# Optimization experiments

Measured on AMD Instinct MI355X. Metric: run time of the kernel, lower is better.

## Reference

```python
import jax, jax.numpy as jnp
import numpy as np

N_DETS = 50000
DEG = 32
N_EDGES = N_DETS * DEG

def _xavier(key, fan_in, fan_out):
    lim = np.sqrt(6.0 / (fan_in + fan_out)).astype(np.float32)
    return jax.random.uniform(key, (fan_in, fan_out), jnp.float32, -lim, lim)

def setup_inputs() -> dict:
    key = jax.random.key(0)
    ks = jax.random.split(key, 10)
    detFeatures = jax.random.normal(ks[0], (N_DETS, 128), jnp.float32)
    # every detection has exactly DEG neighbor pairs -> sorted segment ids, no empty segments
    cIdxs = jnp.repeat(jnp.arange(N_DETS, dtype=jnp.int64), DEG)
    nIdxs = jax.random.randint(ks[1], (N_EDGES,), 0, N_DETS, jnp.int64)
    pairFeatures = jax.random.normal(ks[2], (N_EDGES, 32), jnp.float32)
    return {
        "detFeatures": detFeatures,
        "cIdxs": cIdxs,
        "nIdxs": nIdxs,
        "pairFeatures": pairFeatures,
        "W_fc1": _xavier(ks[3], 128, 32), "b_fc1": jnp.zeros((32,), jnp.float32),
        "W_pw1": _xavier(ks[4], 96, 64), "b_pw1": jnp.zeros((64,), jnp.float32),
        "W_pw2": _xavier(ks[5], 64, 64), "b_pw2": jnp.zeros((64,), jnp.float32),
        "W_pm1": _xavier(ks[6], 64, 64), "b_pm1": jnp.zeros((64,), jnp.float32),
        "W_pm2": _xavier(ks[7], 64, 64), "b_pm2": jnp.zeros((64,), jnp.float32),
        "W_out": _xavier(ks[8], 64, 128), "b_out": jnp.zeros((128,), jnp.float32),
    }

def reference(detFeatures, cIdxs, nIdxs, pairFeatures,
              W_fc1, b_fc1, W_pw1, b_pw1, W_pw2, b_pw2,
              W_pm1, b_pm1, W_pm2, b_pm2, W_out, b_out):
    relu = jax.nn.relu
    # fc1: [N,128] -> [N,32]
    h = relu(detFeatures @ W_fc1 + b_fc1)
    # gather center / neighbor feats per pair; zero neighbor feats on identity rows
    cFeats = h[cIdxs]                                   # [E,32]
    nFeats = jnp.where((cIdxs == nIdxs)[:, None], 0.0, h[nIdxs])  # [E,32]
    x = jnp.concatenate((pairFeatures, cFeats, nFeats), axis=1)   # [E,96]
    x = relu(x @ W_pw1 + b_pw1)                         # [E,64]
    x = relu(x @ W_pw2 + b_pw2)                         # [E,64]
    # per-detection segment max (replaces the O(N) python loop)
    m = jax.ops.segment_max(x, cIdxs, num_segments=detFeatures.shape[0])  # [N,64]
    m = relu(m @ W_pm1 + b_pm1)
    m = relu(m @ W_pm2 + b_pm2)
    refined = m @ W_out + b_out                         # [N,128]
    return relu(detFeatures + refined)
```

## Files before the change

kernel.cpp:

```cpp
#include <hip/hip_runtime.h>

#define NDET 50000
#define DEG 32
#define NEDGE (NDET * DEG)
#define NGROUP (NEDGE / 64)

typedef __attribute__((ext_vector_type(8))) short short8;
typedef __attribute__((ext_vector_type(4))) float f32x4;

__device__ inline unsigned short f2bf(float x) {
    return (unsigned short)((__builtin_bit_cast(unsigned int, x) + 0x8000u) >> 16);
}

__device__ inline short8 pack8(float4 a, float4 b) {
    short8 r;
    r[0] = (short)f2bf(a.x); r[1] = (short)f2bf(a.y);
    r[2] = (short)f2bf(a.z); r[3] = (short)f2bf(a.w);
    r[4] = (short)f2bf(b.x); r[5] = (short)f2bf(b.y);
    r[6] = (short)f2bf(b.z); r[7] = (short)f2bf(b.w);
    return r;
}

__global__ __launch_bounds__(256, 4) void fc1_kernel(
    const float* __restrict__ detF,
    const float* __restrict__ W,
    const float* __restrict__ b,
    unsigned short* __restrict__ hbf)
{
    __shared__ __align__(16) unsigned short WT[32 * 136];

    const int tid  = threadIdx.x;
    const int lane = tid & 63;
    const int wv   = tid >> 6;
    const int m16  = lane & 15;
    const int q    = lane >> 4;

    for (int i = tid; i < 32 * 128; i += 256) {
        int n = i >> 7, k = i & 127;
        WT[n * 136 + k] = f2bf(W[k * 32 + n]);
    }
    __syncthreads();

    const int g = blockIdx.x * 4 + wv;
    if (g >= (NDET + 63) / 64) return;
    const int d0 = g * 64;

    f32x4 acc[4][2];
#pragma unroll
    for (int nt = 0; nt < 2; nt++) {
        float c0 = b[nt * 16 + m16];
#pragma unroll
        for (int mt = 0; mt < 4; mt++) acc[mt][nt] = (f32x4){c0, c0, c0, c0};
    }

#pragma unroll
    for (int ks = 0; ks < 4; ks++) {
#pragma unroll
        for (int mt = 0; mt < 4; mt++) {
            int row = d0 + mt * 16 + m16;
            if (row >= NDET) row = NDET - 1;
            const float* pr = detF + (size_t)row * 128 + ks * 32 + q * 8;
            short8 a = pack8(*(const float4*)pr, *(const float4*)(pr + 4));
#pragma unroll
            for (int nt = 0; nt < 2; nt++) {
                short8 bf = *(const short8*)&WT[(nt * 16 + m16) * 136 + ks * 32 + q * 8];
                acc[mt][nt] = __builtin_amdgcn_mfma_f32_16x16x32_bf16(a, bf, acc[mt][nt], 0, 0, 0);
            }
        }
    }

#pragma unroll
    for (int mt = 0; mt < 4; mt++)
#pragma unroll
        for (int r = 0; r < 4; r++) {
            int row = d0 + mt * 16 + q * 4 + r;
            if (row < NDET) {
#pragma unroll
                for (int nt = 0; nt < 2; nt++)
                    hbf[(size_t)row * 32 + nt * 16 + m16] = f2bf(fmaxf(acc[mt][nt][r], 0.0f));
            }
        }
}

__global__ __launch_bounds__(256, 3) void edge_kernel(
    const unsigned short* __restrict__ hbf,
    const int* __restrict__ nIdx,
    const float* __restrict__ pairF,
    const float* __restrict__ W1,
    const float* __restrict__ b1,
    const float* __restrict__ W2,
    const float* __restrict__ b2,
    unsigned short* __restrict__ m_bf)
{
    __shared__ __align__(16) unsigned short Y1s[4][64 * 72];
    __shared__ __align__(16) unsigned short W2T[64 * 72];

    const int tid  = threadIdx.x;
    const int lane = tid & 63;
    const int wv   = tid >> 6;
    const int m16  = lane & 15;
    const int q    = lane >> 4;

    unsigned short* st = &Y1s[0][0];
    for (int i = tid; i < 64 * 96; i += 256) {
        int n = i / 96, k = i - n * 96;
        st[i] = f2bf(W1[k * 64 + n]);
    }
    for (int i = tid; i < 64 * 64; i += 256) {
        int n = i >> 6, k = i & 63;
        W2T[n * 72 + k] = f2bf(W2[k * 64 + n]);
    }
    __syncthreads();

    short8 w1f[3][4];
#pragma unroll
    for (int nt = 0; nt < 4; nt++) {
        const unsigned short* base = &st[(nt * 16 + m16) * 96];
        w1f[0][nt] = *(const short8*)&base[q * 8];
        w1f[1][nt] = *(const short8*)&base[64 + q * 8];
        w1f[2][nt] = *(const short8*)&base[32 + q * 8];
    }
    float b1r[4], b2r[4];
#pragma unroll
    for (int nt = 0; nt < 4; nt++) {
        b1r[nt] = b1[nt * 16 + m16];
        b2r[nt] = b2[nt * 16 + m16];
    }
    __syncthreads();

    unsigned short* Y1w = &Y1s[wv][0];

    const int wstride = (int)gridDim.x * 4;
    int g = blockIdx.x * 4 + wv;
    if (g >= NGROUP) return;

    int    ni[4];
    float4 pv[4][2];
    short8 nb[4];
    short8 cf2[2];

#define PREF(gg)                                                                  \
    {                                                                             \
        const int E0p = (gg) * 64, d0p = (gg) * 2;                                \
        _Pragma("unroll")                                                         \
        for (int mt = 0; mt < 4; mt++) {                                          \
            int e = E0p + mt * 16 + m16;                                          \
            ni[mt] = nIdx[e];                                                     \
            const float* pr = pairF + (size_t)e * 32 + q * 8;                     \
            pv[mt][0] = *(const float4*)pr;                                       \
            pv[mt][1] = *(const float4*)(pr + 4);                                 \
            nb[mt] = *(const short8*)&hbf[(size_t)ni[mt] * 32 + q * 8];           \
        }                                                                         \
        cf2[0] = *(const short8*)&hbf[(size_t)d0p * 32 + q * 8];                  \
        cf2[1] = *(const short8*)&hbf[(size_t)(d0p + 1) * 32 + q * 8];            \
    }

    PREF(g);
    const short8 zr = {0, 0, 0, 0, 0, 0, 0, 0};

    while (true) {
        const int d0 = g * 2;
        short8 ap[4], an[4], ac[4];
#pragma unroll
        for (int mt = 0; mt < 4; mt++) {
            ap[mt] = pack8(pv[mt][0], pv[mt][1]);
            an[mt] = (ni[mt] == d0 + (mt >> 1)) ? zr : nb[mt];
            ac[mt] = cf2[mt >> 1];
        }
        const int gn = g + wstride;
        const bool more = (gn < NGROUP);
        PREF(more ? gn : g);

        f32x4 acc[4][4];
#pragma unroll
        for (int mt = 0; mt < 4; mt++)
#pragma unroll
            for (int nt = 0; nt < 4; nt++) {
                float c0 = b1r[nt];
                acc[mt][nt] = (f32x4){c0, c0, c0, c0};
            }
#pragma unroll
        for (int mt = 0; mt < 4; mt++)
#pragma unroll
            for (int nt = 0; nt < 4; nt++) {
                acc[mt][nt] = __builtin_amdgcn_mfma_f32_16x16x32_bf16(ap[mt], w1f[0][nt], acc[mt][nt], 0, 0, 0);
                acc[mt][nt] = __builtin_amdgcn_mfma_f32_16x16x32_bf16(an[mt], w1f[1][nt], acc[mt][nt], 0, 0, 0);
                acc[mt][nt] = __builtin_amdgcn_mfma_f32_16x16x32_bf16(ac[mt], w1f[2][nt], acc[mt][nt], 0, 0, 0);
            }

#pragma unroll
        for (int mt = 0; mt < 4; mt++)
#pragma unroll
            for (int nt = 0; nt < 4; nt++)
#pragma unroll
                for (int r = 0; r < 4; r++)
                    Y1w[(mt * 16 + q * 4 + r) * 72 + nt * 16 + m16] =
                        f2bf(fmaxf(acc[mt][nt][r], 0.0f));

        f32x4 acc2[4][4];
#pragma unroll
        for (int mt = 0; mt < 4; mt++)
#pragma unroll
            for (int nt = 0; nt < 4; nt++) {
                float c0 = b2r[nt];
                acc2[mt][nt] = (f32x4){c0, c0, c0, c0};
            }
#pragma unroll
        for (int ks = 0; ks < 2; ks++) {
            short8 af[4];
#pragma unroll
            for (int mt = 0; mt < 4; mt++)
                af[mt] = *(const short8*)&Y1w[(mt * 16 + m16) * 72 + ks * 32 + q * 8];
#pragma unroll
            for (int nt = 0; nt < 4; nt++) {
                short8 wf = *(const short8*)&W2T[(nt * 16 + m16) * 72 + ks * 32 + q * 8];
#pragma unroll
                for (int mt = 0; mt < 4; mt++)
                    acc2[mt][nt] = __builtin_amdgcn_mfma_f32_16x16x32_bf16(af[mt], wf, acc2[mt][nt], 0, 0, 0);
            }
        }

#pragma unroll
        for (int d = 0; d < 2; d++)
#pragma unroll
            for (int nt = 0; nt < 4; nt++) {
                float v = 0.0f;
#pragma unroll
                for (int mt = 2 * d; mt < 2 * d + 2; mt++)
#pragma unroll
                    for (int r = 0; r < 4; r++) v = fmaxf(v, acc2[mt][nt][r]);
                v = fmaxf(v, __shfl_xor(v, 16));
                v = fmaxf(v, __shfl_xor(v, 32));
                if (q == 0) m_bf[(size_t)(d0 + d) * 64 + nt * 16 + m16] = f2bf(v);
            }

        if (!more) break;
        g = gn;
    }
#undef PREF
}

__global__ __launch_bounds__(256, 2) void tail_kernel(
    const float* __restrict__ detF,
    const unsigned short* __restrict__ m_bf,
    const float* __restrict__ Wm1, const float* __restrict__ bm1,
    const float* __restrict__ Wm2, const float* __restrict__ bm2,
    const float* __restrict__ Wo,  const float* __restrict__ bo,
    float* __restrict__ out)
{
    __shared__ __align__(16) unsigned short W1T[64 * 72];
    __shared__ __align__(16) unsigned short W2T[64 * 72];
    __shared__ __align__(16) unsigned short WoT[128 * 72];
    __shared__ __align__(16) unsigned short Tt[4][64 * 72];

    const int tid  = threadIdx.x;
    const int lane = tid & 63;
    const int wv   = tid >> 6;
    const int m16  = lane & 15;
    const int q    = lane >> 4;

    for (int i = tid; i < 64 * 64; i += 256) {
        int n = i >> 6, k = i & 63;
        W1T[n * 72 + k] = f2bf(Wm1[k * 64 + n]);
        W2T[n * 72 + k] = f2bf(Wm2[k * 64 + n]);
    }
    for (int i = tid; i < 128 * 64; i += 256) {
        int n = i >> 6, k = i & 63;
        WoT[n * 72 + k] = f2bf(Wo[k * 128 + n]);
    }
    __syncthreads();

    float bm1r[4], bm2r[4], bor[8];
#pragma unroll
    for (int nt = 0; nt < 4; nt++) {
        bm1r[nt] = bm1[nt * 16 + m16];
        bm2r[nt] = bm2[nt * 16 + m16];
    }
#pragma unroll
    for (int nt = 0; nt < 8; nt++) bor[nt] = bo[nt * 16 + m16];

    unsigned short* Tw = &Tt[wv][0];
    const int NTG = (NDET + 63) / 64;

    for (int gI = blockIdx.x * 4 + wv; gI < NTG; gI += (int)gridDim.x * 4) {
        const int d0 = gI * 64;

        f32x4 acc[4][4];
#pragma unroll
        for (int mt = 0; mt < 4; mt++)
#pragma unroll
            for (int nt = 0; nt < 4; nt++) {
                float c0 = bm1r[nt];
                acc[mt][nt] = (f32x4){c0, c0, c0, c0};
            }
#pragma unroll
        for (int ks = 0; ks < 2; ks++) {
            short8 af[4];
#pragma unroll
            for (int mt = 0; mt < 4; mt++) {
                int row = d0 + mt * 16 + m16;
                if (row >= NDET) row = NDET - 1;
                af[mt] = *(const short8*)&m_bf[(size_t)row * 64 + ks * 32 + q * 8];
            }
#pragma unroll
            for (int mt = 0; mt < 4; mt++)
#pragma unroll
                for (int nt = 0; nt < 4; nt++) {
                    short8 bf = *(const short8*)&W1T[(nt * 16 + m16) * 72 + ks * 32 + q * 8];
                    acc[mt][nt] = __builtin_amdgcn_mfma_f32_16x16x32_bf16(af[mt], bf, acc[mt][nt], 0, 0, 0);
                }
        }
#pragma unroll
        for (int mt = 0; mt < 4; mt++)
#pragma unroll
            for (int nt = 0; nt < 4; nt++)
#pragma unroll
                for (int r = 0; r < 4; r++)
                    Tw[(mt * 16 + q * 4 + r) * 72 + nt * 16 + m16] =
                        f2bf(fmaxf(acc[mt][nt][r], 0.0f));

#pragma unroll
        for (int mt = 0; mt < 4; mt++)
#pragma unroll
            for (int nt = 0; nt < 4; nt++) {
                float c0 = bm2r[nt];
                acc[mt][nt] = (f32x4){c0, c0, c0, c0};
            }
#pragma unroll
        for (int ks = 0; ks < 2; ks++) {
            short8 af[4];
#pragma unroll
            for (int mt = 0; mt < 4; mt++)
                af[mt] = *(const short8*)&Tw[(mt * 16 + m16) * 72 + ks * 32 + q * 8];
#pragma unroll
            for (int mt = 0; mt < 4; mt++)
#pragma unroll
                for (int nt = 0; nt < 4; nt++) {
                    short8 bf = *(const short8*)&W2T[(nt * 16 + m16) * 72 + ks * 32 + q * 8];
                    acc[mt][nt] = __builtin_amdgcn_mfma_f32_16x16x32_bf16(af[mt], bf, acc[mt][nt], 0, 0, 0);
                }
        }
#pragma unroll
        for (int mt = 0; mt < 4; mt++)
#pragma unroll
            for (int nt = 0; nt < 4; nt++)
#pragma unroll
                for (int r = 0; r < 4; r++)
                    Tw[(mt * 16 + q * 4 + r) * 72 + nt * 16 + m16] =
                        f2bf(fmaxf(acc[mt][nt][r], 0.0f));

        short8 a3[4][2];
#pragma unroll
        for (int ks = 0; ks < 2; ks++)
#pragma unroll
            for (int mt = 0; mt < 4; mt++)
                a3[mt][ks] = *(const short8*)&Tw[(mt * 16 + m16) * 72 + ks * 32 + q * 8];

#pragma unroll
        for (int h2 = 0; h2 < 2; h2++) {
            f32x4 acc3[4][4];
#pragma unroll
            for (int mt = 0; mt < 4; mt++)
#pragma unroll
                for (int nt = 0; nt < 4; nt++) {
                    float c0 = bor[h2 * 4 + nt];
                    acc3[mt][nt] = (f32x4){c0, c0, c0, c0};
                }
#pragma unroll
            for (int ks = 0; ks < 2; ks++)
#pragma unroll
                for (int mt = 0; mt < 4; mt++)
#pragma unroll
                    for (int nt = 0; nt < 4; nt++) {
                        short8 bf = *(const short8*)&WoT[((h2 * 4 + nt) * 16 + m16) * 72 + ks * 32 + q * 8];
                        acc3[mt][nt] = __builtin_amdgcn_mfma_f32_16x16x32_bf16(a3[mt][ks], bf, acc3[mt][nt], 0, 0, 0);
                    }
#pragma unroll
            for (int mt = 0; mt < 4; mt++)
#pragma unroll
                for (int r = 0; r < 4; r++) {
                    int row = d0 + mt * 16 + q * 4 + r;
                    if (row < NDET) {
#pragma unroll
                        for (int nt = 0; nt < 4; nt++) {
                            int col = (h2 * 4 + nt) * 16 + m16;
                            float v = detF[(size_t)row * 128 + col] + acc3[mt][nt][r];
                            out[(size_t)row * 128 + col] = fmaxf(v, 0.0f);
                        }
                    }
                }
        }
    }
}

extern "C" void kernel_launch(void* const* d_in, const int* in_sizes, int n_in,
                              void* d_out, int out_size, void* d_ws, size_t ws_size,
                              hipStream_t stream)
{
    const float* detF  = (const float*)d_in[0];
    const int*   nIdx  = (const int*)d_in[2];
    const float* pairF = (const float*)d_in[3];
    const float* W_fc1 = (const float*)d_in[4];
    const float* b_fc1 = (const float*)d_in[5];
    const float* W_pw1 = (const float*)d_in[6];
    const float* b_pw1 = (const float*)d_in[7];
    const float* W_pw2 = (const float*)d_in[8];
    const float* b_pw2 = (const float*)d_in[9];
    const float* W_pm1 = (const float*)d_in[10];
    const float* b_pm1 = (const float*)d_in[11];
    const float* W_pm2 = (const float*)d_in[12];
    const float* b_pm2 = (const float*)d_in[13];
    const float* W_out = (const float*)d_in[14];
    const float* b_out = (const float*)d_in[15];
    float* out = (float*)d_out;

    unsigned short* hbf  = (unsigned short*)d_ws;
    unsigned short* m_bf = hbf + (size_t)NDET * 32;

    fc1_kernel<<<(NDET + 255) / 256, 256, 0, stream>>>(detF, W_fc1, b_fc1, hbf);
    edge_kernel<<<768, 256, 0, stream>>>(hbf, nIdx, pairF,
                                         W_pw1, b_pw1, W_pw2, b_pw2, m_bf);
    tail_kernel<<<256, 256, 0, stream>>>(detF, m_bf, W_pm1, b_pm1, W_pm2, b_pm2,
                                         W_out, b_out, out);
}
```

Measured before the change: 458.7 us.

## Prefetch neighbor indices two iterations ahead and use nontemporal streaming loads

The edge kernel now loads neighbor indices two groups ahead, so the dependent gather of neighbor features for the next group no longer waits on an index load issued in the same prefetch step. This breaks the index-then-gather latency chain. Streamed inputs (pairFeatures, nIdx, detFeatures) are read with nontemporal loads so they do not crowd the gathered hbf table out of cache. The cost is extra registers for the rotating index buffers, which could reduce occupancy.

```diff
diff --git a/kernel.cpp b/kernel.cpp
--- a/kernel.cpp
+++ b/kernel.cpp
@@ -12,14 +12,20 @@
     return (unsigned short)((__builtin_bit_cast(unsigned int, x) + 0x8000u) >> 16);
 }
 
-__device__ inline short8 pack8(float4 a, float4 b) {
+__device__ inline short8 pack8(f32x4 a, f32x4 b) {
     short8 r;
-    r[0] = (short)f2bf(a.x); r[1] = (short)f2bf(a.y);
-    r[2] = (short)f2bf(a.z); r[3] = (short)f2bf(a.w);
-    r[4] = (short)f2bf(b.x); r[5] = (short)f2bf(b.y);
-    r[6] = (short)f2bf(b.z); r[7] = (short)f2bf(b.w);
+    r[0] = (short)f2bf(a[0]); r[1] = (short)f2bf(a[1]);
+    r[2] = (short)f2bf(a[2]); r[3] = (short)f2bf(a[3]);
+    r[4] = (short)f2bf(b[0]); r[5] = (short)f2bf(b[1]);
+    r[6] = (short)f2bf(b[2]); r[7] = (short)f2bf(b[3]);
     return r;
 }
+
+__device__ inline f32x4 nt4(const float* p) {
+    return __builtin_nontemporal_load((const f32x4*)p);
+}
+__device__ inline int ntI(const int* p) { return __builtin_nontemporal_load(p); }
+__device__ inline float ntF(const float* p) { return __builtin_nontemporal_load(p); }
 
 __global__ __launch_bounds__(256, 4) void fc1_kernel(
     const float* __restrict__ detF,
@@ -60,7 +66,7 @@
             int row = d0 + mt * 16 + m16;
             if (row >= NDET) row = NDET - 1;
             const float* pr = detF + (size_t)row * 128 + ks * 32 + q * 8;
-            short8 a = pack8(*(const float4*)pr, *(const float4*)(pr + 4));
+            short8 a = pack8(nt4(pr), nt4(pr + 4));
 #pragma unroll
             for (int nt = 0; nt < 2; nt++) {
                 short8 bf = *(const short8*)&WT[(nt * 16 + m16) * 136 + ks * 32 + q * 8];
@@ -134,29 +140,34 @@
     int g = blockIdx.x * 4 + wv;
     if (g >= NGROUP) return;
 
-    int    ni[4];
-    float4 pv[4][2];
+    int    ni_cur[4], ni_next[4];
+    f32x4  pv[4][2];
     short8 nb[4];
     short8 cf2[2];
-
-#define PREF(gg)                                                                  \
-    {                                                                             \
-        const int E0p = (gg) * 64, d0p = (gg) * 2;                                \
-        _Pragma("unroll")                                                         \
-        for (int mt = 0; mt < 4; mt++) {                                          \
-            int e = E0p + mt * 16 + m16;                                          \
-            ni[mt] = nIdx[e];                                                     \
-            const float* pr = pairF + (size_t)e * 32 + q * 8;                     \
-            pv[mt][0] = *(const float4*)pr;                                       \
-            pv[mt][1] = *(const float4*)(pr + 4);                                 \
-            nb[mt] = *(const short8*)&hbf[(size_t)ni[mt] * 32 + q * 8];           \
-        }                                                                         \
-        cf2[0] = *(const short8*)&hbf[(size_t)d0p * 32 + q * 8];                  \
-        cf2[1] = *(const short8*)&hbf[(size_t)(d0p + 1) * 32 + q * 8];            \
-    }
-
-    PREF(g);
     const short8 zr = {0, 0, 0, 0, 0, 0, 0, 0};
+
+    {
+        const int E0 = g * 64, d0 = g * 2;
+#pragma unroll
+        for (int mt = 0; mt < 4; mt++)
+            ni_cur[mt] = ntI(&nIdx[E0 + mt * 16 + m16]);
+#pragma unroll
+        for (int mt = 0; mt < 4; mt++) {
+            const float* pr = pairF + (size_t)(E0 + mt * 16 + m16) * 32 + q * 8;
+            pv[mt][0] = nt4(pr);
+            pv[mt][1] = nt4(pr + 4);
+        }
+#pragma unroll
+        for (int mt = 0; mt < 4; mt++)
+            nb[mt] = *(const short8*)&hbf[(size_t)ni_cur[mt] * 32 + q * 8];
+        cf2[0] = *(const short8*)&hbf[(size_t)d0 * 32 + q * 8];
+        cf2[1] = *(const short8*)&hbf[(size_t)(d0 + 1) * 32 + q * 8];
+        const int g1 = g + wstride;
+        const int gs = (g1 < NGROUP) ? g1 : g;
+#pragma unroll
+        for (int mt = 0; mt < 4; mt++)
+            ni_next[mt] = ntI(&nIdx[gs * 64 + mt * 16 + m16]);
+    }
 
     while (true) {
         const int d0 = g * 2;
@@ -164,12 +175,29 @@
 #pragma unroll
         for (int mt = 0; mt < 4; mt++) {
             ap[mt] = pack8(pv[mt][0], pv[mt][1]);
-            an[mt] = (ni[mt] == d0 + (mt >> 1)) ? zr : nb[mt];
+            an[mt] = (ni_cur[mt] == d0 + (mt >> 1)) ? zr : nb[mt];
             ac[mt] = cf2[mt >> 1];
         }
-        const int gn = g + wstride;
-        const bool more = (gn < NGROUP);
-        PREF(more ? gn : g);
+
+        const int g1 = g + wstride;
+        const bool more = (g1 < NGROUP);
+        const int gn = more ? g1 : g;
+        const int g2 = g1 + wstride;
+        const int gf = (g2 < NGROUP) ? g2 : gn;
+
+        int ni_far[4];
+#pragma unroll
+        for (int mt = 0; mt < 4; mt++)
+            ni_far[mt] = ntI(&nIdx[gf * 64 + mt * 16 + m16]);
+#pragma unroll
+        for (int mt = 0; mt < 4; mt++) {
+            const float* pr = pairF + (size_t)(gn * 64 + mt * 16 + m16) * 32 + q * 8;
+            pv[mt][0] = nt4(pr);
+            pv[mt][1] = nt4(pr + 4);
+            nb[mt] = *(const short8*)&hbf[(size_t)ni_next[mt] * 32 + q * 8];
+        }
+        cf2[0] = *(const short8*)&hbf[(size_t)(gn * 2) * 32 + q * 8];
+        cf2[1] = *(const short8*)&hbf[(size_t)(gn * 2 + 1) * 32 + q * 8];
 
         f32x4 acc[4][4];
 #pragma unroll
@@ -235,9 +263,13 @@
             }
 
         if (!more) break;
-        g = gn;
-    }
-#undef PREF
+#pragma unroll
+        for (int mt = 0; mt < 4; mt++) {
+            ni_cur[mt]  = ni_next[mt];
+            ni_next[mt] = ni_far[mt];
+        }
+        g = g1;
+    }
 }
 
 __global__ __launch_bounds__(256, 2) void tail_kernel(
@@ -384,7 +416,7 @@
 #pragma unroll
                         for (int nt = 0; nt < 4; nt++) {
                             int col = (h2 * 4 + nt) * 16 + m16;
-                            float v = detF[(size_t)row * 128 + col] + acc3[mt][nt][r];
+                            float v = ntF(&detF[(size_t)row * 128 + col]) + acc3[mt][nt][r];
                             out[(size_t)row * 128 + col] = fmaxf(v, 0.0f);
                         }
                     }
```

Result: slower. 483.3 us (+5.4%).
